# Kernel tuning notes

Hardware: AMD Instinct MI355X
Metric: run time of the kernel (lower is better)

The kernel has to match this reference:

```python
import jax, jax.numpy as jnp
import numpy as np
import math

B, S, D, H = 2, 2048, 768, 12
HD = D // H


def setup_inputs() -> dict:
    key = jax.random.key(0)
    ks = jax.random.split(key, 9)
    scale = 1.0 / math.sqrt(D)
    x = jax.random.normal(ks[0], (B, S, D), dtype=jnp.float32)
    # causal mask: True where attention is allowed (query i attends to key j<=i)
    mask = jnp.tril(jnp.ones((S, S), dtype=bool))[None, None]  # [1,1,S,S]
    wq = jax.random.normal(ks[1], (D, D), dtype=jnp.float32) * scale
    bq = jnp.zeros((D,), dtype=jnp.float32)
    wk = jax.random.normal(ks[2], (D, D), dtype=jnp.float32) * scale
    bk = jnp.zeros((D,), dtype=jnp.float32)
    wv = jax.random.normal(ks[3], (D, D), dtype=jnp.float32) * scale
    bv = jnp.zeros((D,), dtype=jnp.float32)
    wo = jax.random.normal(ks[4], (D, D), dtype=jnp.float32) * scale
    bo = jnp.zeros((D,), dtype=jnp.float32)
    return {"x": x, "mask": mask, "wq": wq, "bq": bq, "wk": wk, "bk": bk,
            "wv": wv, "bv": bv, "wo": wo, "bo": bo}


def reference(x, mask, wq, bq, wk, bk, wv, bv, wo, bo):
    b, s, d = x.shape
    # projections (flax Linear: y = x @ kernel + bias)
    q = (x @ wq + bq).reshape(b, s, H, HD).transpose(0, 2, 1, 3)  # [b,h,s,hd]
    k = (x @ wk + bk).reshape(b, s, H, HD).transpose(0, 2, 1, 3)
    v = (x @ wv + bv).reshape(b, s, H, HD).transpose(0, 2, 1, 3)
    scores = jnp.einsum('bhqd,bhkd->bhqk', q, k) / math.sqrt(HD)  # [b,h,s,s]
    scores = jnp.where(mask, scores, -jnp.inf)
    attn = jax.nn.softmax(scores, axis=-1)
    out = jnp.einsum('bhqk,bhkd->bhqd', attn, v)  # [b,h,s,hd]
    out = out.transpose(0, 2, 1, 3).reshape(b, s, d)
    return out @ wo + bo
```

## Files before the change

kernel.cpp:

```cpp
#include <hip/hip_runtime.h>
#include <math.h>

#define BATCH 2
#define SEQ   2048
#define DMODEL 768
#define NHEAD 12
#define HDIM  64

typedef unsigned short u16;
typedef __attribute__((ext_vector_type(8))) short bf16x8;
typedef __attribute__((ext_vector_type(4))) float f32x4;
typedef __attribute__((ext_vector_type(16))) float f32x16;
typedef __attribute__((ext_vector_type(8))) unsigned short us8;
typedef __attribute__((ext_vector_type(4))) unsigned short us4;

__device__ __forceinline__ u16 f2bf(float f) {
    union { float f; unsigned u; } v; v.f = f;
    unsigned u = v.u;
    u += 0x7fff + ((u >> 16) & 1);
    return (u16)(u >> 16);
}

__device__ __forceinline__ float fexp2(float x) {
#if __has_builtin(__builtin_amdgcn_exp2f)
    return __builtin_amdgcn_exp2f(x);
#else
    return exp2f(x);
#endif
}

__device__ __forceinline__ void g2l16(const void* g, void* l) {
    __builtin_amdgcn_global_load_lds(
        (const __attribute__((address_space(1))) unsigned int*)g,
        (__attribute__((address_space(3))) unsigned int*)(unsigned int)(unsigned long long)(uintptr_t)l,
        16, 0, 0);
}

__device__ __forceinline__ void stage_rows(const u16* g, u16* lds, int nrows,
                                           int tid) {
    const int row = tid >> 2, col = (tid & 3) * 8;
    g2l16(g + (size_t)row * DMODEL + col, lds + tid * 8);
    if (nrows == 128) {
        g2l16(g + (size_t)(row + 64) * DMODEL + col, lds + 2048 + tid * 8);
    } else if (nrows == 96) {
        if (tid < 128)
            g2l16(g + (size_t)(row + 64) * DMODEL + col, lds + 2048 + tid * 8);
    }
}

__global__ __launch_bounds__(256) void prep(const float* __restrict__ x,
                                            const float* __restrict__ w0,
                                            const float* __restrict__ w1,
                                            const float* __restrict__ w2,
                                            const float* __restrict__ w3,
                                            u16* __restrict__ xb,
                                            u16* __restrict__ Wt_all) {
    __shared__ float t[32][33];
    const int bid = blockIdx.x;
    if (bid < 3072) {
        int i = bid * 256 + threadIdx.x;
        float4 v = ((const float4*)x)[i];
        us4 o;
        o.x = f2bf(v.x); o.y = f2bf(v.y); o.z = f2bf(v.z); o.w = f2bf(v.w);
        *(us4*)&xb[(size_t)i * 4] = o;
    } else {
        const int wid = bid - 3072;
        const int z  = wid / 576;
        const int rr = wid % 576;
        const int by = rr / 24, bx = rr % 24;
        const float* W = z == 0 ? w0 : z == 1 ? w1 : z == 2 ? w2 : w3;
        u16* Wt = Wt_all + (size_t)z * DMODEL * DMODEL;

        int tx = threadIdx.x & 31, ty = threadIdx.x >> 5;
        int xg = bx * 32 + tx;
        #pragma unroll
        for (int j = 0; j < 32; j += 8)
            t[ty + j][tx] = W[(size_t)(by * 32 + ty + j) * DMODEL + xg];
        __syncthreads();
        int x2 = by * 32 + tx;
        #pragma unroll
        for (int j = 0; j < 32; j += 8)
            Wt[(size_t)(bx * 32 + ty + j) * DMODEL + x2] = f2bf(t[tx][ty + j]);
    }
}

__global__ __launch_bounds__(256) void gemm_qkv(
    const u16* __restrict__ xb, const u16* __restrict__ WtQK,
    const u16* __restrict__ WtV,
    const float* __restrict__ bq, const float* __restrict__ bk,
    const float* __restrict__ bv,
    u16* __restrict__ QK, u16* __restrict__ Vt) {

    __shared__ __align__(16) u16 As[128 * 32];
    __shared__ __align__(16) u16 Bs[128 * 32];

    const int tid  = threadIdx.x;
    const int lane = tid & 63;
    const int w    = tid >> 6;
    const int quad = lane >> 4, l16 = lane & 15;
    const int wm   = w >> 1, wn = w & 1;
    const int b    = blockIdx.x;

    if (b < 512) {
        const int m0 = (b >> 4) * 128;
        const int n0 = (b & 15) * 96;
        f32x4 acc[4][3] = {};
        for (int k0 = 0; k0 < DMODEL; k0 += 32) {
            stage_rows(xb   + (size_t)m0 * DMODEL + k0, As, 128, tid);
            stage_rows(WtQK + (size_t)n0 * DMODEL + k0, Bs,  96, tid);
            __syncthreads();
            bf16x8 af[4], bfr[3];
            #pragma unroll
            for (int i = 0; i < 4; ++i)
                af[i] = *(const bf16x8*)&As[(wm * 64 + i * 16 + l16) * 32 + quad * 8];
            #pragma unroll
            for (int j = 0; j < 3; ++j)
                bfr[j] = *(const bf16x8*)&Bs[(wn * 48 + j * 16 + l16) * 32 + quad * 8];
            #pragma unroll
            for (int i = 0; i < 4; ++i)
                #pragma unroll
                for (int j = 0; j < 3; ++j)
                    acc[i][j] = __builtin_amdgcn_mfma_f32_16x16x32_bf16(af[i], bfr[j], acc[i][j], 0, 0, 0);
            __syncthreads();
        }
        const size_t n_elem = (size_t)BATCH * SEQ * DMODEL;
        #pragma unroll
        for (int j = 0; j < 3; ++j) {
            const int n     = n0 + wn * 48 + j * 16 + l16;
            const int which = n / 768;
            const int nn    = n - which * 768;
            const float bias  = (which == 0 ? bq : bk)[nn];
            const float scale = (which == 0) ? 0.18033688011112043f : 1.0f;
            const int h = nn >> 6, hd = nn & 63;
            u16* outw = QK + (size_t)which * n_elem;
            #pragma unroll
            for (int i = 0; i < 4; ++i) {
                const int mbase = m0 + wm * 64 + i * 16 + quad * 4;
                #pragma unroll
                for (int r = 0; r < 4; ++r) {
                    const int m  = mbase + r;
                    const int b_ = m >> 11, s_ = m & 2047;
                    outw[(size_t)((b_ * NHEAD + h) * SEQ + s_) * HDIM + hd] =
                        f2bf((acc[i][j][r] + bias) * scale);
                }
            }
        }
    } else {
        const int vj = b - 512;
        const int m0 = (vj & 7) * 96;
        const int n0 = (vj >> 3) * 128;
        f32x4 acc[3][4] = {};
        for (int k0 = 0; k0 < DMODEL; k0 += 32) {
            stage_rows(WtV + (size_t)m0 * DMODEL + k0, As,  96, tid);
            stage_rows(xb  + (size_t)n0 * DMODEL + k0, Bs, 128, tid);
            __syncthreads();
            bf16x8 af[3], bfr[4];
            #pragma unroll
            for (int i = 0; i < 3; ++i)
                af[i] = *(const bf16x8*)&As[(wm * 48 + i * 16 + l16) * 32 + quad * 8];
            #pragma unroll
            for (int j = 0; j < 4; ++j)
                bfr[j] = *(const bf16x8*)&Bs[(wn * 64 + j * 16 + l16) * 32 + quad * 8];
            #pragma unroll
            for (int i = 0; i < 3; ++i)
                #pragma unroll
                for (int j = 0; j < 4; ++j)
                    acc[i][j] = __builtin_amdgcn_mfma_f32_16x16x32_bf16(af[i], bfr[j], acc[i][j], 0, 0, 0);
            __syncthreads();
        }
        #pragma unroll
        for (int i = 0; i < 3; ++i) {
            const int rbase = m0 + wm * 48 + i * 16 + quad * 4;
            #pragma unroll
            for (int r = 0; r < 4; ++r) {
                const int row_g = rbase + r;
                const float bias = bv[row_g];
                const int h = row_g >> 6, hd = row_g & 63;
                #pragma unroll
                for (int j = 0; j < 4; ++j) {
                    const int col_g = n0 + wn * 64 + j * 16 + l16;
                    const int b_ = col_g >> 11, s_ = col_g & 2047;
                    Vt[(size_t)((b_ * NHEAD + h) * HDIM + hd) * SEQ + s_] =
                        f2bf(acc[i][j][r] + bias);
                }
            }
        }
    }
}

__global__ __launch_bounds__(256) void gemm_out(
    const u16* __restrict__ Ag, const u16* __restrict__ Bt,
    const float* __restrict__ bo, float* __restrict__ out) {

    __shared__ __align__(16) u16 As[64 * 32];
    __shared__ __align__(16) u16 Bs[64 * 32];

    const int tid  = threadIdx.x;
    const int lane = tid & 63;
    const int w    = tid >> 6;
    const int quad = lane >> 4, l16 = lane & 15;
    const int wm   = w >> 1, wn = w & 1;
    const int m0 = blockIdx.x * 64, n0 = blockIdx.y * 64;

    const int rowA = tid >> 2;
    const int kch  = (tid & 3) * 8;

    f32x4 acc[2][2] = {};

    for (int k0 = 0; k0 < DMODEL; k0 += 32) {
        g2l16(Ag + (size_t)(m0 + rowA) * DMODEL + k0 + kch, As + tid * 8);
        g2l16(Bt + (size_t)(n0 + rowA) * DMODEL + k0 + kch, Bs + tid * 8);
        __syncthreads();

        bf16x8 af[2], bfr[2];
        #pragma unroll
        for (int i = 0; i < 2; ++i)
            af[i] = *(const bf16x8*)&As[(wm * 32 + i * 16 + l16) * 32 + quad * 8];
        #pragma unroll
        for (int j = 0; j < 2; ++j)
            bfr[j] = *(const bf16x8*)&Bs[(wn * 32 + j * 16 + l16) * 32 + quad * 8];
        #pragma unroll
        for (int i = 0; i < 2; ++i)
            #pragma unroll
            for (int j = 0; j < 2; ++j)
                acc[i][j] = __builtin_amdgcn_mfma_f32_16x16x32_bf16(af[i], bfr[j], acc[i][j], 0, 0, 0);
        __syncthreads();
    }

    #pragma unroll
    for (int i = 0; i < 2; ++i) {
        const int mbase = m0 + wm * 32 + i * 16 + quad * 4;
        #pragma unroll
        for (int r = 0; r < 4; ++r) {
            const int m = mbase + r;
            #pragma unroll
            for (int j = 0; j < 2; ++j) {
                const int n = n0 + wn * 32 + j * 16 + l16;
                out[(size_t)m * DMODEL + n] = acc[i][j][r] + bo[n];
            }
        }
    }
}

__global__ __launch_bounds__(256) void flash_attn_mfma(
    const u16* __restrict__ Q, const u16* __restrict__ K,
    const u16* __restrict__ Vt, u16* __restrict__ A) {

    __shared__ __align__(16) u16 Kl[3][64 * 64];
    __shared__ __align__(16) u16 Vl[3][64 * 64];

    const int tid  = threadIdx.x;
    const int lane = tid & 63;
    const int w    = tid >> 6;
    const int l32  = lane & 31;
    const int hi   = lane >> 5;
    const int qh   = w & 1;
    const int kh   = w >> 1;

    const int sid = 767 - (int)blockIdx.x;
    const int j   = sid / 24;
    const int bh  = sid - j * 24;
    const int tc  = j + 1;

    const size_t base = (size_t)bh * SEQ * HDIM;
    const u16* Qg = Q + base;
    const u16* Kg = K + base;
    const u16* Vg = Vt + base;

    const int wq0 = j * 64 + qh * 32;
    const int qg  = wq0 + l32;

    bf16x8 qf[4];
    #pragma unroll
    for (int c = 0; c < 4; ++c)
        qf[c] = *(const bf16x8*)&Qg[(size_t)qg * 64 + 16 * c + 8 * hi];

    f32x16 o0 = {}, o1 = {};
    float l_acc = 0.f;

    const int ch0 = tid, ch1 = tid + 256;
    const int r0 = ch0 >> 3, lc0 = (ch0 & 7) ^ (r0 & 7);
    const int r1 = ch1 >> 3, lc1 = (ch1 & 7) ^ (r1 & 7);
    const u16* kp0 = Kg + (size_t)r0 * 64 + lc0 * 8;
    const u16* kp1 = Kg + (size_t)r1 * 64 + lc1 * 8;
    const u16* vp0 = Vg + (size_t)r0 * SEQ + lc0 * 8;
    const u16* vp1 = Vg + (size_t)r1 * SEQ + lc1 * 8;

    auto STAGE = [&](int buf) {
        g2l16(kp0, &Kl[buf][ch0 * 8]);
        g2l16(kp1, &Kl[buf][ch1 * 8]);
        g2l16(vp0, &Vl[buf][ch0 * 8]);
        g2l16(vp1, &Vl[buf][ch1 * 8]);
        kp0 += 64 * 64; kp1 += 64 * 64;
        vp0 += 64;      vp1 += 64;
    };

    STAGE(0);
    if (tc > 1) STAGE(1);

    int cur = 0, nb = 2;
    const int cx = l32 & 7;
    for (int t = 0; t < tc; ++t) {
        if (t + 1 < tc) asm volatile("s_waitcnt vmcnt(4)" ::: "memory");
        else            asm volatile("s_waitcnt vmcnt(0)" ::: "memory");
        __builtin_amdgcn_s_barrier();
        if (t + 2 < tc) { STAGE(nb); nb = (nb == 2) ? 0 : nb + 1; }

        const bool live = !(t == tc - 1 && qh == 0 && kh == 1);
        if (live) {
            const u16* Kc = Kl[cur];
            const u16* Vc = Vl[cur];
            const int j0 = t * 64;

            f32x16 s = {};
            __builtin_amdgcn_s_setprio(1);
            #pragma unroll
            for (int c = 0; c < 4; ++c) {
                bf16x8 kf = *(const bf16x8*)&Kc[(32 * kh + l32) * 64 + (((2 * c + hi) ^ cx) * 8)];
                s = __builtin_amdgcn_mfma_f32_32x32x16_bf16(kf, qf[c], s, 0, 0, 0);
            }
            __builtin_amdgcn_s_setprio(0);

            if (t == tc - 1) {
                #pragma unroll
                for (int r = 0; r < 16; ++r) {
                    const int key = j0 + 32 * kh + (r & 3) + 8 * (r >> 2) + 4 * hi;
                    if (key > qg) s[r] = -INFINITY;
                }
            }

            #pragma unroll
            for (int r = 0; r < 16; ++r) s[r] = fexp2(s[r]);
            float ps = 0.f;
            #pragma unroll
            for (int r = 0; r < 16; ++r) ps += s[r];
            l_acc += ps;

            bf16x8 pa[2];
            #pragma unroll
            for (int kw = 0; kw < 2; ++kw) {
                const int m0i = 2 * kw;
                unsigned a0l, a0h, a1l, a1h;
                asm("v_cvt_pk_bf16_f32 %0, %1, %2" : "=v"(a0l) : "v"(s[4 * m0i + 0]), "v"(s[4 * m0i + 1]));
                asm("v_cvt_pk_bf16_f32 %0, %1, %2" : "=v"(a0h) : "v"(s[4 * m0i + 2]), "v"(s[4 * m0i + 3]));
                asm("v_cvt_pk_bf16_f32 %0, %1, %2" : "=v"(a1l) : "v"(s[4 * (m0i + 1) + 0]), "v"(s[4 * (m0i + 1) + 1]));
                asm("v_cvt_pk_bf16_f32 %0, %1, %2" : "=v"(a1h) : "v"(s[4 * (m0i + 1) + 2]), "v"(s[4 * (m0i + 1) + 3]));
                asm("v_permlane32_swap_b32 %0, %1" : "+v"(a0l), "+v"(a1l));
                asm("v_permlane32_swap_b32 %0, %1" : "+v"(a0h), "+v"(a1h));
                union { unsigned u[4]; bf16x8 v; } pu;
                pu.u[0] = a0l; pu.u[1] = a0h; pu.u[2] = a1l; pu.u[3] = a1h;
                pa[kw] = pu.v;
            }

            __builtin_amdgcn_s_setprio(1);
            #pragma unroll
            for (int kw = 0; kw < 2; ++kw) {
                const int lc = ((4 * kh + 2 * kw + hi) ^ cx) * 8;
                bf16x8 vf0 = *(const bf16x8*)&Vc[l32 * 64 + lc];
                bf16x8 vf1 = *(const bf16x8*)&Vc[(32 + l32) * 64 + lc];
                o0 = __builtin_amdgcn_mfma_f32_32x32x16_bf16(vf0, pa[kw], o0, 0, 0, 0);
                o1 = __builtin_amdgcn_mfma_f32_32x32x16_bf16(vf1, pa[kw], o1, 0, 0, 0);
            }
            __builtin_amdgcn_s_setprio(0);
        }

        cur = (cur == 2) ? 0 : cur + 1;
    }

    l_acc += __shfl_xor(l_acc, 32);

    __syncthreads();

    float* ob = (float*)Kl;
    float* lb = (float*)Vl;
    if (kh == 1) {
        #pragma unroll
        for (int r = 0; r < 16; ++r) {
            ob[qh * 2048 + r * 64 + lane]        = o0[r];
            ob[qh * 2048 + (16 + r) * 64 + lane] = o1[r];
        }
        lb[qh * 64 + lane] = l_acc;
    }
    __syncthreads();

    if (kh == 0) {
        #pragma unroll
        for (int r = 0; r < 16; ++r) {
            o0[r] += ob[qh * 2048 + r * 64 + lane];
            o1[r] += ob[qh * 2048 + (16 + r) * 64 + lane];
        }
        const float inv = 1.0f / (l_acc + lb[qh * 64 + lane]);

        u16* Ot = ((u16*)Vl) + 256 + qh * 2304;
        #pragma unroll
        for (int r = 0; r < 16; ++r) {
            const int d = (r & 3) + 8 * (r >> 2) + 4 * hi;
            Ot[l32 * 72 + d]      = f2bf(o0[r] * inv);
            Ot[l32 * 72 + 32 + d] = f2bf(o1[r] * inv);
        }
        const int row = lane >> 1, d0 = (lane & 1) * 32;
        const int b_ = bh / NHEAD, h_ = bh % NHEAD;
        u16* dst = A + ((size_t)(b_ * SEQ + wq0 + row)) * DMODEL + h_ * HDIM + d0;
        #pragma unroll
        for (int k2 = 0; k2 < 4; ++k2)
            *(us8*)&dst[k2 * 8] = *(const us8*)&Ot[row * 72 + d0 + k2 * 8];
    }
}

extern "C" void kernel_launch(void* const* d_in, const int* in_sizes, int n_in,
                              void* d_out, int out_size, void* d_ws, size_t ws_size,
                              hipStream_t stream) {
    const float* x  = (const float*)d_in[0];
    const float* wq = (const float*)d_in[2];
    const float* bq = (const float*)d_in[3];
    const float* wk = (const float*)d_in[4];
    const float* bk = (const float*)d_in[5];
    const float* wv = (const float*)d_in[6];
    const float* bv = (const float*)d_in[7];
    const float* wo = (const float*)d_in[8];
    const float* bo = (const float*)d_in[9];
    float* out = (float*)d_out;

    const size_t n_elem = (size_t)BATCH * SEQ * DMODEL;
    const size_t w_elem = (size_t)DMODEL * DMODEL;

    u16* xb     = (u16*)d_ws;
    u16* Wt_all = xb + n_elem;
    u16* Qw     = Wt_all + 4 * w_elem;
    u16* Vtw    = Qw + 2 * n_elem;
    u16* Aw     = Vtw + n_elem;

    dim3 blk(256);

    prep<<<dim3(3072 + 2304), blk, 0, stream>>>(x, wq, wk, wv, wo, xb, Wt_all);

    gemm_qkv<<<dim3(768), blk, 0, stream>>>(xb, Wt_all, Wt_all + 2 * w_elem,
                                            bq, bk, bv, Qw, Vtw);

    flash_attn_mfma<<<dim3(768), blk, 0, stream>>>(Qw, Qw + n_elem, Vtw, Aw);

    gemm_out<<<dim3(64, 12), blk, 0, stream>>>(Aw, Wt_all + 3 * w_elem, bo, out);
}
```

Measured before the change: 159.9 us.

## Triple-buffer LDS staging in projection GEMMs with async global-to-LDS prefetch

Both projection GEMMs now stage A and B tiles into a three-deep LDS ring using global_load_lds. Tiles are prefetched two iterations ahead, and explicit vmcnt waits plus a single barrier replace the two __syncthreads per k-step, so loads overlap MFMA work. Per-thread global pointers are precomputed and advanced by 32 each step. The flash-attention block-to-tile mapping is also changed so the middle third of blocks runs in ascending rather than descending order. This rebalances causal work across the grid. The cost is more LDS per block and hand-tuned waitcnt counts that must match the number of loads each wave issues.

```diff
diff --git a/kernel.cpp b/kernel.cpp
--- a/kernel.cpp
+++ b/kernel.cpp
@@ -34,18 +34,6 @@
         (const __attribute__((address_space(1))) unsigned int*)g,
         (__attribute__((address_space(3))) unsigned int*)(unsigned int)(unsigned long long)(uintptr_t)l,
         16, 0, 0);
-}
-
-__device__ __forceinline__ void stage_rows(const u16* g, u16* lds, int nrows,
-                                           int tid) {
-    const int row = tid >> 2, col = (tid & 3) * 8;
-    g2l16(g + (size_t)row * DMODEL + col, lds + tid * 8);
-    if (nrows == 128) {
-        g2l16(g + (size_t)(row + 64) * DMODEL + col, lds + 2048 + tid * 8);
-    } else if (nrows == 96) {
-        if (tid < 128)
-            g2l16(g + (size_t)(row + 64) * DMODEL + col, lds + 2048 + tid * 8);
-    }
 }
 
 __global__ __launch_bounds__(256) void prep(const float* __restrict__ x,
@@ -91,8 +79,7 @@
     const float* __restrict__ bv,
     u16* __restrict__ QK, u16* __restrict__ Vt) {
 
-    __shared__ __align__(16) u16 As[128 * 32];
-    __shared__ __align__(16) u16 Bs[128 * 32];
+    __shared__ __align__(16) u16 Sb[3][224 * 32];
 
     const int tid  = threadIdx.x;
     const int lane = tid & 63;
@@ -100,15 +87,48 @@
     const int quad = lane >> 4, l16 = lane & 15;
     const int wm   = w >> 1, wn = w & 1;
     const int b    = blockIdx.x;
-
-    if (b < 512) {
-        const int m0 = (b >> 4) * 128;
-        const int n0 = (b & 15) * 96;
+    const bool qk  = b < 512;
+
+    const int m0 = qk ? (b >> 4) * 128 : (((b - 512) & 7) * 96);
+    const int n0 = qk ? (b & 15) * 96  : (((b - 512) >> 3) * 128);
+
+    auto rowbase = [&](int row) -> const u16* {
+        if (qk) return row < 128 ? xb   + (size_t)(m0 + row) * DMODEL
+                                 : WtQK + (size_t)(n0 + row - 128) * DMODEL;
+        return row < 96 ? WtV + (size_t)(m0 + row) * DMODEL
+                        : xb  + (size_t)(n0 + row - 96) * DMODEL;
+    };
+    const int c0 = tid, c1 = tid + 256, c2 = tid + 512, c3 = (tid & 127) + 768;
+    const u16* gp0 = rowbase(c0 >> 2) + (c0 & 3) * 8;
+    const u16* gp1 = rowbase(c1 >> 2) + (c1 & 3) * 8;
+    const u16* gp2 = rowbase(c2 >> 2) + (c2 & 3) * 8;
+    const u16* gp3 = rowbase(c3 >> 2) + (c3 & 3) * 8;
+    const bool four = tid < 128;
+
+    auto STAGE = [&](int buf) {
+        u16* L = Sb[buf];
+        g2l16(gp0, L + c0 * 8);
+        g2l16(gp1, L + c1 * 8);
+        g2l16(gp2, L + c2 * 8);
+        if (four) g2l16(gp3, L + c3 * 8);
+        gp0 += 32; gp1 += 32; gp2 += 32; gp3 += 32;
+    };
+
+    STAGE(0); STAGE(1);
+    int cur = 0, nb = 2;
+
+    if (qk) {
         f32x4 acc[4][3] = {};
-        for (int k0 = 0; k0 < DMODEL; k0 += 32) {
-            stage_rows(xb   + (size_t)m0 * DMODEL + k0, As, 128, tid);
-            stage_rows(WtQK + (size_t)n0 * DMODEL + k0, Bs,  96, tid);
-            __syncthreads();
+        for (int it = 0; it < 24; ++it) {
+            if (it < 23) {
+                if (w < 2) asm volatile("s_waitcnt vmcnt(4)" ::: "memory");
+                else       asm volatile("s_waitcnt vmcnt(3)" ::: "memory");
+            } else         asm volatile("s_waitcnt vmcnt(0)" ::: "memory");
+            __builtin_amdgcn_s_barrier();
+            if (it < 22) { STAGE(nb); nb = nb == 2 ? 0 : nb + 1; }
+
+            const u16* As = Sb[cur];
+            const u16* Bs = Sb[cur] + 128 * 32;
             bf16x8 af[4], bfr[3];
             #pragma unroll
             for (int i = 0; i < 4; ++i)
@@ -121,7 +141,7 @@
                 #pragma unroll
                 for (int j = 0; j < 3; ++j)
                     acc[i][j] = __builtin_amdgcn_mfma_f32_16x16x32_bf16(af[i], bfr[j], acc[i][j], 0, 0, 0);
-            __syncthreads();
+            cur = cur == 2 ? 0 : cur + 1;
         }
         const size_t n_elem = (size_t)BATCH * SEQ * DMODEL;
         #pragma unroll
@@ -146,14 +166,17 @@
             }
         }
     } else {
-        const int vj = b - 512;
-        const int m0 = (vj & 7) * 96;
-        const int n0 = (vj >> 3) * 128;
         f32x4 acc[3][4] = {};
-        for (int k0 = 0; k0 < DMODEL; k0 += 32) {
-            stage_rows(WtV + (size_t)m0 * DMODEL + k0, As,  96, tid);
-            stage_rows(xb  + (size_t)n0 * DMODEL + k0, Bs, 128, tid);
-            __syncthreads();
+        for (int it = 0; it < 24; ++it) {
+            if (it < 23) {
+                if (w < 2) asm volatile("s_waitcnt vmcnt(4)" ::: "memory");
+                else       asm volatile("s_waitcnt vmcnt(3)" ::: "memory");
+            } else         asm volatile("s_waitcnt vmcnt(0)" ::: "memory");
+            __builtin_amdgcn_s_barrier();
+            if (it < 22) { STAGE(nb); nb = nb == 2 ? 0 : nb + 1; }
+
+            const u16* As = Sb[cur];
+            const u16* Bs = Sb[cur] + 96 * 32;
             bf16x8 af[3], bfr[4];
             #pragma unroll
             for (int i = 0; i < 3; ++i)
@@ -166,7 +189,7 @@
                 #pragma unroll
                 for (int j = 0; j < 4; ++j)
                     acc[i][j] = __builtin_amdgcn_mfma_f32_16x16x32_bf16(af[i], bfr[j], acc[i][j], 0, 0, 0);
-            __syncthreads();
+            cur = cur == 2 ? 0 : cur + 1;
         }
         #pragma unroll
         for (int i = 0; i < 3; ++i) {
@@ -192,8 +215,7 @@
     const u16* __restrict__ Ag, const u16* __restrict__ Bt,
     const float* __restrict__ bo, float* __restrict__ out) {
 
-    __shared__ __align__(16) u16 As[64 * 32];
-    __shared__ __align__(16) u16 Bs[64 * 32];
+    __shared__ __align__(16) u16 Sb[3][128 * 32];
 
     const int tid  = threadIdx.x;
     const int lane = tid & 63;
@@ -202,16 +224,32 @@
     const int wm   = w >> 1, wn = w & 1;
     const int m0 = blockIdx.x * 64, n0 = blockIdx.y * 64;
 
-    const int rowA = tid >> 2;
-    const int kch  = (tid & 3) * 8;
+    const int c0 = tid, c1 = tid + 256;
+    auto rowbase = [&](int row) -> const u16* {
+        return row < 64 ? Ag + (size_t)(m0 + row) * DMODEL
+                        : Bt + (size_t)(n0 + row - 64) * DMODEL;
+    };
+    const u16* gp0 = rowbase(c0 >> 2) + (c0 & 3) * 8;
+    const u16* gp1 = rowbase(c1 >> 2) + (c1 & 3) * 8;
+
+    auto STAGE = [&](int buf) {
+        g2l16(gp0, Sb[buf] + c0 * 8);
+        g2l16(gp1, Sb[buf] + c1 * 8);
+        gp0 += 32; gp1 += 32;
+    };
+
+    STAGE(0); STAGE(1);
+    int cur = 0, nb = 2;
 
     f32x4 acc[2][2] = {};
-
-    for (int k0 = 0; k0 < DMODEL; k0 += 32) {
-        g2l16(Ag + (size_t)(m0 + rowA) * DMODEL + k0 + kch, As + tid * 8);
-        g2l16(Bt + (size_t)(n0 + rowA) * DMODEL + k0 + kch, Bs + tid * 8);
-        __syncthreads();
-
+    for (int it = 0; it < 24; ++it) {
+        if (it < 23) asm volatile("s_waitcnt vmcnt(2)" ::: "memory");
+        else         asm volatile("s_waitcnt vmcnt(0)" ::: "memory");
+        __builtin_amdgcn_s_barrier();
+        if (it < 22) { STAGE(nb); nb = nb == 2 ? 0 : nb + 1; }
+
+        const u16* As = Sb[cur];
+        const u16* Bs = Sb[cur] + 64 * 32;
         bf16x8 af[2], bfr[2];
         #pragma unroll
         for (int i = 0; i < 2; ++i)
@@ -224,7 +262,7 @@
             #pragma unroll
             for (int j = 0; j < 2; ++j)
                 acc[i][j] = __builtin_amdgcn_mfma_f32_16x16x32_bf16(af[i], bfr[j], acc[i][j], 0, 0, 0);
-        __syncthreads();
+        cur = cur == 2 ? 0 : cur + 1;
     }
 
     #pragma unroll
@@ -257,7 +295,8 @@
     const int qh   = w & 1;
     const int kh   = w >> 1;
 
-    const int sid = 767 - (int)blockIdx.x;
+    const int b0  = (int)blockIdx.x;
+    const int sid = ((b0 >> 8) == 1) ? b0 : 767 - b0;
     const int j   = sid / 24;
     const int bh  = sid - j * 24;
     const int tc  = j + 1;
```

Measured after the change: 158.0 us. Within noise of the previous version (-1.2%).
